# Optimization experiments

Hardware: AMD Instinct MI355X
Metric: run time of the kernel (lower is better)

The kernel has to match this reference:

```python
import jax, jax.numpy as jnp
import numpy as np

TOP_K = 2
EPS = 1e-6

def setup_inputs() -> dict:
    key = jax.random.key(0)
    ks = jax.random.split(key, 4)
    B, L, D, E, ED = 2, 2048, 2048, 8, 2048
    scale_gu = (6.0 / D) ** 0.5   # kaiming_uniform-ish bound
    scale_dn = (6.0 / ED) ** 0.5
    return {
        "x": jax.random.normal(ks[0], (B, L, D), jnp.float32),
        "router_scale": jnp.ones((D,), jnp.float32),
        "gate_w": jax.random.normal(ks[1], (D, E), jnp.float32) * (D ** -0.5),
        "gate_up": jax.random.uniform(ks[2], (E, D, 2 * ED), jnp.float32, -scale_gu, scale_gu),
        "down": jax.random.uniform(ks[3], (E, ED, D), jnp.float32, -scale_dn, scale_dn),
        "per_expert_scale": jnp.ones((E,), jnp.float32),
    }

def reference(x, router_scale, gate_w, gate_up, down, per_expert_scale):
    B, L, D = x.shape
    E = gate_up.shape[0]
    # --- Router: RMSNorm (no scale) * D^-0.5 * router_scale -> linear -> softmax -> topk -> renorm
    h = x * jax.lax.rsqrt(jnp.mean(x * x, axis=-1, keepdims=True) + EPS)
    h = h * (D ** -0.5) * router_scale
    logits = (h @ gate_w).astype(jnp.float32)            # [B,L,E]
    probs = jax.nn.softmax(logits, axis=-1)
    w, idx = jax.lax.top_k(probs, TOP_K)                 # [B,L,K]
    w = w / jnp.clip(jnp.sum(w, axis=-1, keepdims=True), 1e-12)
    w = w.astype(x.dtype)
    # --- Experts: dense compute over all experts, weighted combine by routing
    N = B * L
    xf = x.reshape(N, D)
    idxf = idx.reshape(N, TOP_K)
    wf = w.reshape(N, TOP_K)
    # combine[n,e] = sum_k wf[n,k] * (idxf[n,k]==e); top_k indices are distinct per token
    combine = jnp.zeros((N, E), x.dtype).at[jnp.arange(N)[:, None], idxf].add(wf)
    hh = jnp.einsum('nd,edf->nef', xf, gate_up)          # [N,E,2*ED]
    gate, up = jnp.split(hh, 2, axis=-1)
    act = jax.nn.gelu(gate, approximate=False) * up      # [N,E,ED]
    y = jnp.einsum('nef,efd->ned', act, down)            # [N,E,D]
    out = jnp.einsum('ne,ned->nd', combine * per_expert_scale, y)
    return out.reshape(B, L, D)
```

## Files before the change

kernel.cpp:

```cpp
#include <hip/hip_runtime.h>
#include <hip/hip_bf16.h>
#include <math.h>

#define NTOK 4096
#define DM   2048
#define NE   8
#define BK2  32
#define NT   64
#define TILE_BYTES 32768
#define B_OFF      16384

using f32x4  = float __attribute__((ext_vector_type(4)));
using bf16x8 = __bf16 __attribute__((ext_vector_type(8)));
using u32x4  = unsigned int __attribute__((ext_vector_type(4)));

__device__ __forceinline__ unsigned short bf16bits(float f){
  unsigned u = __builtin_bit_cast(unsigned, f);
  return (unsigned short)((u + 0x7fffu + ((u >> 16) & 1u)) >> 16);
}

__device__ __forceinline__ void load_lds16(const void* g, void* l){
  __builtin_amdgcn_global_load_lds(
      (const __attribute__((address_space(1))) unsigned int*)g,
      (__attribute__((address_space(3))) unsigned int*)l, 16, 0, 0);
}

__global__ __launch_bounds__(256) void router_kernel(
    const float* __restrict__ x, const float* __restrict__ rs,
    const float* __restrict__ gw, const float* __restrict__ pes,
    unsigned short* __restrict__ xbf, int* __restrict__ cnt,
    int* __restrict__ toklist, float* __restrict__ slotw)
{
  const int wv = threadIdx.x >> 6, l = threadIdx.x & 63;
  const int n = blockIdx.x * 4 + wv;
  const float* xr = x + (size_t)n * DM;
  unsigned short* xb = xbf + (size_t)n * DM;
  float ssq = 0.f;
  float lg[8] = {0,0,0,0,0,0,0,0};
  #pragma unroll
  for (int q = 0; q < 8; ++q){
    int c4 = l + 64 * q;
    float4 v = ((const float4*)xr)[c4];
    float4 r = ((const float4*)rs)[c4];
    ssq += v.x*v.x + v.y*v.y + v.z*v.z + v.w*v.w;
    ushort4 o; o.x = bf16bits(v.x); o.y = bf16bits(v.y); o.z = bf16bits(v.z); o.w = bf16bits(v.w);
    ((ushort4*)xb)[c4] = o;
    float xs0 = v.x*r.x, xs1 = v.y*r.y, xs2 = v.z*r.z, xs3 = v.w*r.w;
    const float4* gp = (const float4*)(gw + (size_t)c4 * 32);
    float4 ga, gb;
    ga = gp[0]; gb = gp[1];
    lg[0]+=xs0*ga.x; lg[1]+=xs0*ga.y; lg[2]+=xs0*ga.z; lg[3]+=xs0*ga.w;
    lg[4]+=xs0*gb.x; lg[5]+=xs0*gb.y; lg[6]+=xs0*gb.z; lg[7]+=xs0*gb.w;
    ga = gp[2]; gb = gp[3];
    lg[0]+=xs1*ga.x; lg[1]+=xs1*ga.y; lg[2]+=xs1*ga.z; lg[3]+=xs1*ga.w;
    lg[4]+=xs1*gb.x; lg[5]+=xs1*gb.y; lg[6]+=xs1*gb.z; lg[7]+=xs1*gb.w;
    ga = gp[4]; gb = gp[5];
    lg[0]+=xs2*ga.x; lg[1]+=xs2*ga.y; lg[2]+=xs2*ga.z; lg[3]+=xs2*ga.w;
    lg[4]+=xs2*gb.x; lg[5]+=xs2*gb.y; lg[6]+=xs2*gb.z; lg[7]+=xs2*gb.w;
    ga = gp[6]; gb = gp[7];
    lg[0]+=xs3*ga.x; lg[1]+=xs3*ga.y; lg[2]+=xs3*ga.z; lg[3]+=xs3*ga.w;
    lg[4]+=xs3*gb.x; lg[5]+=xs3*gb.y; lg[6]+=xs3*gb.z; lg[7]+=xs3*gb.w;
  }
  #pragma unroll
  for (int off = 32; off; off >>= 1){
    ssq += __shfl_xor(ssq, off, 64);
    #pragma unroll
    for (int e2 = 0; e2 < 8; ++e2) lg[e2] += __shfl_xor(lg[e2], off, 64);
  }
  if (l == 0){
    float c = rsqrtf(ssq * (1.0f/DM) + 1e-6f) * 0.022097086912079608f;
    float mx = -1e30f;
    #pragma unroll
    for (int e2 = 0; e2 < 8; ++e2){ lg[e2] *= c; mx = fmaxf(mx, lg[e2]); }
    float l0 = lg[0]; int i0 = 0;
    #pragma unroll
    for (int e2 = 1; e2 < 8; ++e2) if (lg[e2] > l0){ l0 = lg[e2]; i0 = e2; }
    int i1 = (i0 == 0) ? 1 : 0; float l1 = (i0 == 0) ? lg[1] : lg[0];
    #pragma unroll
    for (int e2 = 0; e2 < 8; ++e2){ if (e2 != i0 && lg[e2] > l1){ l1 = lg[e2]; i1 = e2; } }
    float p0 = expf(l0 - mx), p1 = expf(l1 - mx);
    float sw = fmaxf(p0 + p1, 1e-12f);
    float w0 = p0 / sw, w1 = p1 / sw;
    int s0 = atomicAdd(&cnt[i0], 1);
    toklist[i0 * NTOK + s0] = n;
    slotw[i0 * NTOK + s0] = w0 * pes[i0];
    int s1 = atomicAdd(&cnt[i1], 1);
    toklist[i1 * NTOK + s1] = n;
    slotw[i1 * NTOK + s1] = w1 * pes[i1];
  }
}

__global__ void scan_kernel(const int* __restrict__ cnt, int* __restrict__ basep){
  if (threadIdx.x == 0){
    int a = 0;
    for (int e = 0; e < NE; ++e){ basep[e] = a; a += cnt[e]; }
  }
}

__global__ __launch_bounds__(256) void conv_transpose_kernel(
    const float* __restrict__ W, unsigned short* __restrict__ Wt, int ncols)
{
  const int z = blockIdx.z;
  const float* src = W + (size_t)z * 2048 * ncols;
  unsigned short* dst = Wt + (size_t)z * ncols * 2048;
  const int n0 = blockIdx.x * 64, k0 = blockIdx.y * 64;
  __shared__ __align__(16) unsigned short t[64][72];
  const int tid = threadIdx.x;
  const int kl = tid >> 4;
  const int nl = (tid & 15) * 4;
  #pragma unroll
  for (int q = 0; q < 4; ++q){
    int k = kl + q * 16;
    float4 v = *(const float4*)(src + (size_t)(k0 + k) * ncols + n0 + nl);
    t[nl+0][k] = bf16bits(v.x);
    t[nl+1][k] = bf16bits(v.y);
    t[nl+2][k] = bf16bits(v.z);
    t[nl+3][k] = bf16bits(v.w);
  }
  __syncthreads();
  const int nr = tid >> 3;
  const int k8 = (tid & 7) * 8;
  #pragma unroll
  for (int q = 0; q < 2; ++q){
    int n = nr + q * 32;
    u32x4 v = *(const u32x4*)&t[n][k8];
    *(u32x4*)(dst + (size_t)(n0 + n) * 2048 + k0 + k8) = v;
  }
}

template<int MODE>
__global__ __launch_bounds__(512, 2) void moe_gemm(
    const unsigned short* __restrict__ Abuf,
    const unsigned short* __restrict__ Wt,
    unsigned short* __restrict__ act,
    float* __restrict__ out,
    const int* __restrict__ cnt,
    const int* __restrict__ basep,
    const int* __restrict__ toklist,
    const float* __restrict__ slotw,
    int e0)
{
  const int z = blockIdx.z, e = e0 + z;
  const int ce = cnt[e];
  const int m0 = blockIdx.y * 256;
  if (m0 >= ce) return;
  const int fb = blockIdx.x * (MODE == 0 ? 128 : 256);
  const int tid = threadIdx.x;
  const int l = tid & 63;
  const int wv = tid >> 6;
  const int wr = wv >> 2;
  const int wc = wv & 3;
  const int baseE = basep[e];
  const size_t ncols = (MODE == 0) ? 4096 : 2048;
  const unsigned short* Wz = Wt + (size_t)z * ncols * 2048;

  __shared__ __align__(16) unsigned short smem[4 * TILE_BYTES / 2];

  const unsigned short* asrc[2];
  #pragma unroll
  for (int q = 0; q < 2; ++q){
    int r = q * 128 + (tid >> 2);
    int g = (tid & 3) ^ ((r >> 1) & 3);
    long rsrc;
    if (MODE == 0) rsrc = toklist[e * NTOK + min(m0 + r, ce - 1)];
    else           rsrc = baseE + min(m0 + r, ce - 1);
    asrc[q] = Abuf + (size_t)rsrc * 2048 + g * 8;
  }
  const unsigned short* bsrc[2];
  #pragma unroll
  for (int q = 0; q < 2; ++q){
    int col = q * 128 + (tid >> 2);
    int g = (tid & 3) ^ ((col >> 1) & 3);
    int n;
    if (MODE == 0){ int sub = col & 63; n = fb + (col >> 6) * 32 + (sub & 31) + ((sub & 32) ? 2048 : 0); }
    else n = fb + col;
    bsrc[q] = Wz + (size_t)n * 2048 + g * 8;
  }
  const int ldst = tid * 16;

  const int kq = l >> 4;
  const int swz = (kq ^ (((l & 15) >> 1) & 3)) * 16;
  const int abase = (wr * 128 + (l & 15)) * 64 + swz;
  const int bbase = B_OFF + (wc * 64 + (l & 15)) * 64 + swz;

  f32x4 acc[8][4];
  #pragma unroll
  for (int i = 0; i < 8; ++i)
    #pragma unroll
    for (int j = 0; j < 4; ++j)
      acc[i][j] = (f32x4){0.f, 0.f, 0.f, 0.f};

  auto stage_a = [&](int buf, int st){
    char* base = (char*)smem + buf * TILE_BYTES;
    load_lds16(asrc[0] + st * BK2, base + ldst);
    load_lds16(asrc[1] + st * BK2, base + 8192 + ldst);
  };
  auto stage_b = [&](int buf, int st){
    char* base = (char*)smem + buf * TILE_BYTES + B_OFF;
    load_lds16(bsrc[0] + st * BK2, base + ldst);
    load_lds16(bsrc[1] + st * BK2, base + 8192 + ldst);
  };

  stage_a(0, 0); stage_b(0, 0);
  stage_a(1, 1); stage_b(1, 1);
  stage_a(2, 2); stage_b(2, 2);
  asm volatile("s_waitcnt vmcnt(8)" ::: "memory");
  __builtin_amdgcn_s_barrier();
  asm volatile("" ::: "memory");

  #pragma unroll 1
  for (int kt = 0; kt < NT; ++kt){
    const char* C = (const char*)smem + (kt & 3) * TILE_BYTES;
    const int sb = (kt + 3) & 3;
    const int st = min(kt + 3, NT - 1);
    bf16x8 af[4], bfr[4];
    #pragma unroll
    for (int ni = 0; ni < 4; ++ni) bfr[ni] = *(const bf16x8*)(C + bbase + ni * 1024);
    #pragma unroll
    for (int mi = 0; mi < 4; ++mi) af[mi] = *(const bf16x8*)(C + abase + mi * 1024);
    stage_a(sb, st);
    asm volatile("" ::: "memory");
    __builtin_amdgcn_s_barrier();
    asm volatile("" ::: "memory");
    __builtin_amdgcn_s_setprio(1);
    #pragma unroll
    for (int ni = 0; ni < 4; ++ni)
      #pragma unroll
      for (int mi = 0; mi < 4; ++mi)
        acc[mi][ni] = __builtin_amdgcn_mfma_f32_16x16x32_bf16(af[mi], bfr[ni], acc[mi][ni], 0, 0, 0);
    __builtin_amdgcn_s_setprio(0);
    asm volatile("" ::: "memory");
    __builtin_amdgcn_s_barrier();
    asm volatile("" ::: "memory");
    #pragma unroll
    for (int mi = 0; mi < 4; ++mi) af[mi] = *(const bf16x8*)(C + abase + (mi + 4) * 1024);
    stage_b(sb, st);
    asm volatile("" ::: "memory");
    __builtin_amdgcn_s_barrier();
    asm volatile("" ::: "memory");
    __builtin_amdgcn_s_setprio(1);
    #pragma unroll
    for (int ni = 0; ni < 4; ++ni)
      #pragma unroll
      for (int mi = 0; mi < 4; ++mi)
        acc[mi + 4][ni] = __builtin_amdgcn_mfma_f32_16x16x32_bf16(af[mi], bfr[ni], acc[mi + 4][ni], 0, 0, 0);
    __builtin_amdgcn_s_setprio(0);
    asm volatile("s_waitcnt vmcnt(8)" ::: "memory");
    __builtin_amdgcn_s_barrier();
    asm volatile("" ::: "memory");
  }
  asm volatile("s_waitcnt vmcnt(0)" ::: "memory");

  const int lq4 = (l >> 4) * 4;
  if (MODE == 0){
    #pragma unroll
    for (int mi = 0; mi < 8; ++mi)
      #pragma unroll
      for (int j = 0; j < 4; ++j){
        int s = m0 + wr * 128 + mi * 16 + lq4 + j;
        if (s < ce){
          size_t rowb = (size_t)(baseE + s) * 2048;
          #pragma unroll
          for (int p = 0; p < 2; ++p){
            float g = acc[mi][p][j];
            float u = acc[mi][p + 2][j];
            float a = 0.5f * g * (1.0f + erff(g * 0.70710678118654752f)) * u;
            act[rowb + fb + wc * 32 + p * 16 + (l & 15)] = bf16bits(a);
          }
        }
      }
  } else {
    #pragma unroll
    for (int mi = 0; mi < 8; ++mi)
      #pragma unroll
      for (int j = 0; j < 4; ++j){
        int s = m0 + wr * 128 + mi * 16 + lq4 + j;
        if (s < ce){
          int tokn = toklist[e * NTOK + s];
          float wgt = slotw[e * NTOK + s];
          float* orow = out + (size_t)tokn * 2048 + fb + wc * 64 + (l & 15);
          #pragma unroll
          for (int ni = 0; ni < 4; ++ni)
            atomicAdd(&orow[ni * 16], wgt * acc[mi][ni][j]);
        }
      }
  }
}

extern "C" void kernel_launch(void* const* d_in, const int* in_sizes, int n_in,
                              void* d_out, int out_size, void* d_ws, size_t ws_size,
                              hipStream_t stream)
{
  const float* x   = (const float*)d_in[0];
  const float* rs  = (const float*)d_in[1];
  const float* gw  = (const float*)d_in[2];
  const float* w1  = (const float*)d_in[3];
  const float* w2  = (const float*)d_in[4];
  const float* pes = (const float*)d_in[5];
  float* out = (float*)d_out;

  char* ws = (char*)d_ws;
  int*   cnt     = (int*)ws;
  int*   basep   = (int*)(ws + 64);
  int*   toklist = (int*)(ws + 256);
  float* slotw   = (float*)(ws + 256 + (size_t)NE * NTOK * 4);
  unsigned short* xbf = (unsigned short*)(ws + 256 + 2 * (size_t)NE * NTOK * 4);
  unsigned short* act = xbf + (size_t)NTOK * DM;
  unsigned short* wtb = act + (size_t)2 * NTOK * DM;

  const size_t fixed = (size_t)((char*)wtb - ws);
  const size_t per_e = (size_t)4096 * 2048 * 2;
  int EG = NE;
  while (EG > 1 && fixed + (size_t)EG * per_e > ws_size) EG >>= 1;

  hipMemsetAsync(d_out, 0, (size_t)out_size * sizeof(float), stream);
  hipMemsetAsync(cnt, 0, 64, stream);
  router_kernel<<<NTOK / 4, 256, 0, stream>>>(x, rs, gw, pes, xbf, cnt, toklist, slotw);
  scan_kernel<<<1, 64, 0, stream>>>(cnt, basep);

  for (int g = 0; g < NE; g += EG){
    conv_transpose_kernel<<<dim3(64, 32, EG), 256, 0, stream>>>(
        w1 + (size_t)g * 2048 * 4096, wtb, 4096);
    moe_gemm<0><<<dim3(16, 16, EG), 512, 0, stream>>>(
        xbf, wtb, act, out, cnt, basep, toklist, slotw, g);
  }
  for (int g = 0; g < NE; g += EG){
    conv_transpose_kernel<<<dim3(32, 32, EG), 256, 0, stream>>>(
        w2 + (size_t)g * 2048 * 2048, wtb, 2048);
    moe_gemm<1><<<dim3(8, 16, EG), 512, 0, stream>>>(
        act, wtb, act, out, cnt, basep, toklist, slotw, g);
  }
}
```

Baseline: 564.9 us.

## Replace atomic scatter output with bf16 staging buffer and separate combine kernel

The down-projection GEMM used to atomically add weighted fp32 results into the output. It now writes bf16 per-slot rows to a staging buffer, and a new combine kernel gathers each token's two expert rows through a token-to-slot map. This removes the output memset and the float atomics, at the cost of an extra bf16 round trip and lower precision in y. The change also remaps block indices so blocks are spread across XCDs, relaxes launch bounds to one block per CU, and replaces memory clobbers with sched_barrier around the barriers.

After: 574.8 us. About the same (+1.8%).

```diff
diff --git a/kernel.cpp b/kernel.cpp
--- a/kernel.cpp
+++ b/kernel.cpp
@@ -14,6 +14,9 @@
 using bf16x8 = __bf16 __attribute__((ext_vector_type(8)));
 using u32x4  = unsigned int __attribute__((ext_vector_type(4)));
 
+#define SBAR()  __builtin_amdgcn_s_barrier()
+#define SCHED() __builtin_amdgcn_sched_barrier(0)
+
 __device__ __forceinline__ unsigned short bf16bits(float f){
   unsigned u = __builtin_bit_cast(unsigned, f);
   return (unsigned short)((u + 0x7fffu + ((u >> 16) & 1u)) >> 16);
@@ -29,7 +32,8 @@
     const float* __restrict__ x, const float* __restrict__ rs,
     const float* __restrict__ gw, const float* __restrict__ pes,
     unsigned short* __restrict__ xbf, int* __restrict__ cnt,
-    int* __restrict__ toklist, float* __restrict__ slotw)
+    int* __restrict__ toklist, float* __restrict__ slotw,
+    int* __restrict__ tok2slot)
 {
   const int wv = threadIdx.x >> 6, l = threadIdx.x & 63;
   const int n = blockIdx.x * 4 + wv;
@@ -84,9 +88,11 @@
     int s0 = atomicAdd(&cnt[i0], 1);
     toklist[i0 * NTOK + s0] = n;
     slotw[i0 * NTOK + s0] = w0 * pes[i0];
+    tok2slot[2 * n] = (i0 << 16) | s0;
     int s1 = atomicAdd(&cnt[i1], 1);
     toklist[i1 * NTOK + s1] = n;
     slotw[i1 * NTOK + s1] = w1 * pes[i1];
+    tok2slot[2 * n + 1] = (i1 << 16) | s1;
   }
 }
 
@@ -129,22 +135,29 @@
 }
 
 template<int MODE>
-__global__ __launch_bounds__(512, 2) void moe_gemm(
+__global__ __launch_bounds__(512, 1) void moe_gemm(
     const unsigned short* __restrict__ Abuf,
     const unsigned short* __restrict__ Wt,
     unsigned short* __restrict__ act,
-    float* __restrict__ out,
+    unsigned short* __restrict__ ybuf,
     const int* __restrict__ cnt,
     const int* __restrict__ basep,
     const int* __restrict__ toklist,
-    const float* __restrict__ slotw,
     int e0)
 {
-  const int z = blockIdx.z, e = e0 + z;
+  const int gx = gridDim.x, gy = gridDim.y, gz = gridDim.z;
+  int flat = blockIdx.x + gx * (blockIdx.y + gy * blockIdx.z);
+  int per  = (gx * gy * gz) >> 3;
+  int id2  = (flat & 7) * per + (flat >> 3);
+  int fpb  = gy * gz;
+  int fbi  = id2 / fpb;
+  int rem  = id2 % fpb;
+  const int z  = rem / gy;
+  const int e  = e0 + z;
   const int ce = cnt[e];
-  const int m0 = blockIdx.y * 256;
+  const int m0 = (rem % gy) * 256;
   if (m0 >= ce) return;
-  const int fb = blockIdx.x * (MODE == 0 ? 128 : 256);
+  const int fb = fbi * (MODE == 0 ? 128 : 256);
   const int tid = threadIdx.x;
   const int l = tid & 63;
   const int wv = tid >> 6;
@@ -204,9 +217,10 @@
   stage_a(0, 0); stage_b(0, 0);
   stage_a(1, 1); stage_b(1, 1);
   stage_a(2, 2); stage_b(2, 2);
-  asm volatile("s_waitcnt vmcnt(8)" ::: "memory");
-  __builtin_amdgcn_s_barrier();
-  asm volatile("" ::: "memory");
+  asm volatile("s_waitcnt vmcnt(8)");
+  SCHED();
+  SBAR();
+  SCHED();
 
   #pragma unroll 1
   for (int kt = 0; kt < NT; ++kt){
@@ -219,9 +233,9 @@
     #pragma unroll
     for (int mi = 0; mi < 4; ++mi) af[mi] = *(const bf16x8*)(C + abase + mi * 1024);
     stage_a(sb, st);
-    asm volatile("" ::: "memory");
-    __builtin_amdgcn_s_barrier();
-    asm volatile("" ::: "memory");
+    SCHED();
+    SBAR();
+    SCHED();
     __builtin_amdgcn_s_setprio(1);
     #pragma unroll
     for (int ni = 0; ni < 4; ++ni)
@@ -229,15 +243,15 @@
       for (int mi = 0; mi < 4; ++mi)
         acc[mi][ni] = __builtin_amdgcn_mfma_f32_16x16x32_bf16(af[mi], bfr[ni], acc[mi][ni], 0, 0, 0);
     __builtin_amdgcn_s_setprio(0);
-    asm volatile("" ::: "memory");
-    __builtin_amdgcn_s_barrier();
-    asm volatile("" ::: "memory");
+    SCHED();
+    SBAR();
+    SCHED();
     #pragma unroll
     for (int mi = 0; mi < 4; ++mi) af[mi] = *(const bf16x8*)(C + abase + (mi + 4) * 1024);
     stage_b(sb, st);
-    asm volatile("" ::: "memory");
-    __builtin_amdgcn_s_barrier();
-    asm volatile("" ::: "memory");
+    SCHED();
+    SBAR();
+    SCHED();
     __builtin_amdgcn_s_setprio(1);
     #pragma unroll
     for (int ni = 0; ni < 4; ++ni)
@@ -245,11 +259,14 @@
       for (int mi = 0; mi < 4; ++mi)
         acc[mi + 4][ni] = __builtin_amdgcn_mfma_f32_16x16x32_bf16(af[mi], bfr[ni], acc[mi + 4][ni], 0, 0, 0);
     __builtin_amdgcn_s_setprio(0);
-    asm volatile("s_waitcnt vmcnt(8)" ::: "memory");
-    __builtin_amdgcn_s_barrier();
-    asm volatile("" ::: "memory");
-  }
-  asm volatile("s_waitcnt vmcnt(0)" ::: "memory");
+    SCHED();
+    asm volatile("s_waitcnt vmcnt(8)");
+    SCHED();
+    SBAR();
+    SCHED();
+  }
+  asm volatile("s_waitcnt vmcnt(0)");
+  SCHED();
 
   const int lq4 = (l >> 4) * 4;
   if (MODE == 0){
@@ -276,14 +293,48 @@
       for (int j = 0; j < 4; ++j){
         int s = m0 + wr * 128 + mi * 16 + lq4 + j;
         if (s < ce){
-          int tokn = toklist[e * NTOK + s];
-          float wgt = slotw[e * NTOK + s];
-          float* orow = out + (size_t)tokn * 2048 + fb + wc * 64 + (l & 15);
+          unsigned short* yr = ybuf + (size_t)(baseE + s) * 2048 + fb + wc * 64 + (l & 15);
           #pragma unroll
           for (int ni = 0; ni < 4; ++ni)
-            atomicAdd(&orow[ni * 16], wgt * acc[mi][ni][j]);
+            yr[ni * 16] = bf16bits(acc[mi][ni][j]);
         }
       }
+  }
+}
+
+__global__ __launch_bounds__(256) void combine_kernel(
+    const unsigned short* __restrict__ ybuf, const int* __restrict__ tok2slot,
+    const float* __restrict__ slotw, const int* __restrict__ basep,
+    float* __restrict__ out)
+{
+  const int n = blockIdx.x * 4 + (threadIdx.x >> 6);
+  const int l = threadIdx.x & 63;
+  int p0 = tok2slot[2 * n], p1 = tok2slot[2 * n + 1];
+  int e0 = p0 >> 16, s0 = p0 & 0xffff;
+  int e1 = p1 >> 16, s1 = p1 & 0xffff;
+  float w0 = slotw[e0 * NTOK + s0], w1 = slotw[e1 * NTOK + s1];
+  const unsigned short* y0 = ybuf + (size_t)(basep[e0] + s0) * 2048;
+  const unsigned short* y1 = ybuf + (size_t)(basep[e1] + s1) * 2048;
+  float* o = out + (size_t)n * 2048;
+  #pragma unroll
+  for (int q = 0; q < 4; ++q){
+    int c8 = (l + 64 * q) * 8;
+    u32x4 a = *(const u32x4*)(y0 + c8);
+    u32x4 b = *(const u32x4*)(y1 + c8);
+    float rr[8];
+    #pragma unroll
+    for (int i = 0; i < 4; ++i){
+      float a0 = __builtin_bit_cast(float, a[i] << 16);
+      float a1 = __builtin_bit_cast(float, a[i] & 0xffff0000u);
+      float b0 = __builtin_bit_cast(float, b[i] << 16);
+      float b1 = __builtin_bit_cast(float, b[i] & 0xffff0000u);
+      rr[2*i]   = w0 * a0 + w1 * b0;
+      rr[2*i+1] = w0 * a1 + w1 * b1;
+    }
+    float4 v0 = {rr[0], rr[1], rr[2], rr[3]};
+    float4 v1 = {rr[4], rr[5], rr[6], rr[7]};
+    *(float4*)(o + c8) = v0;
+    *(float4*)(o + c8 + 4) = v1;
   }
 }
 
@@ -300,34 +351,36 @@
   float* out = (float*)d_out;
 
   char* ws = (char*)d_ws;
-  int*   cnt     = (int*)ws;
-  int*   basep   = (int*)(ws + 64);
-  int*   toklist = (int*)(ws + 256);
-  float* slotw   = (float*)(ws + 256 + (size_t)NE * NTOK * 4);
-  unsigned short* xbf = (unsigned short*)(ws + 256 + 2 * (size_t)NE * NTOK * 4);
-  unsigned short* act = xbf + (size_t)NTOK * DM;
-  unsigned short* wtb = act + (size_t)2 * NTOK * DM;
+  int*   cnt      = (int*)ws;
+  int*   basep    = (int*)(ws + 64);
+  int*   toklist  = (int*)(ws + 256);
+  float* slotw    = (float*)(ws + 256 + (size_t)NE * NTOK * 4);
+  int*   tok2slot = (int*)(ws + 256 + 2 * (size_t)NE * NTOK * 4);
+  unsigned short* xbf  = (unsigned short*)(ws + 256 + 2 * (size_t)NE * NTOK * 4 + (size_t)NTOK * 8);
+  unsigned short* act  = xbf + (size_t)NTOK * DM;
+  unsigned short* ybuf = act + (size_t)2 * NTOK * DM;
+  unsigned short* wtb  = ybuf + (size_t)2 * NTOK * DM;
 
   const size_t fixed = (size_t)((char*)wtb - ws);
   const size_t per_e = (size_t)4096 * 2048 * 2;
   int EG = NE;
   while (EG > 1 && fixed + (size_t)EG * per_e > ws_size) EG >>= 1;
 
-  hipMemsetAsync(d_out, 0, (size_t)out_size * sizeof(float), stream);
   hipMemsetAsync(cnt, 0, 64, stream);
-  router_kernel<<<NTOK / 4, 256, 0, stream>>>(x, rs, gw, pes, xbf, cnt, toklist, slotw);
+  router_kernel<<<NTOK / 4, 256, 0, stream>>>(x, rs, gw, pes, xbf, cnt, toklist, slotw, tok2slot);
   scan_kernel<<<1, 64, 0, stream>>>(cnt, basep);
 
   for (int g = 0; g < NE; g += EG){
     conv_transpose_kernel<<<dim3(64, 32, EG), 256, 0, stream>>>(
         w1 + (size_t)g * 2048 * 4096, wtb, 4096);
     moe_gemm<0><<<dim3(16, 16, EG), 512, 0, stream>>>(
-        xbf, wtb, act, out, cnt, basep, toklist, slotw, g);
+        xbf, wtb, act, ybuf, cnt, basep, toklist, g);
   }
   for (int g = 0; g < NE; g += EG){
     conv_transpose_kernel<<<dim3(32, 32, EG), 256, 0, stream>>>(
         w2 + (size_t)g * 2048 * 2048, wtb, 2048);
     moe_gemm<1><<<dim3(8, 16, EG), 512, 0, stream>>>(
-        act, wtb, act, out, cnt, basep, toklist, slotw, g);
-  }
-}
+        act, wtb, act, ybuf, cnt, basep, toklist, g);
+  }
+  combine_kernel<<<NTOK / 4, 256, 0, stream>>>(ybuf, tok2slot, slotw, basep, out);
+}
```
